# Kernel tuning notes

Measured on AMD Instinct MI355X. Metric: run time of the kernel, lower is better.

Reference implementation:

```python
import jax, jax.numpy as jnp
import numpy as np

B, S, E = 8, 2048, 128
DECAY = 1.2
LN_EPS = 1e-3  # keras LayerNormalization default epsilon


def setup_inputs() -> dict:
    key = jax.random.key(0)
    k1, k2, k3, k4 = jax.random.split(key, 4)
    return {
        "x": jax.random.normal(k1, (B, S, E), dtype=jnp.float32),
        "dense_w": jax.random.normal(k2, (E, E), dtype=jnp.float32) * 0.02,
        "dense_b": jnp.zeros((E,), dtype=jnp.float32),
        "concept_map": jax.random.normal(k3, (E, E, E), dtype=jnp.float32) * 0.02,
        "ln_gamma": jnp.ones((E,), dtype=jnp.float32),
        "ln_beta": jnp.zeros((E,), dtype=jnp.float32),
    }


def reference(x, dense_w, dense_b, concept_map, ln_gamma, ln_beta):
    # Dense projection
    h = x @ dense_w + dense_b  # (B, S, E)
    b, s, e = h.shape

    # Decayed prefix-sum recurrence: s_i = (s_{i-1} + h_{i-1}) / 1.2, s_0 = 0
    def step(carry, xt):
        new = (carry + xt) / DECAY
        return new, new

    h_t = jnp.swapaxes(h, 0, 1)  # (S, B, E)
    _, s_tail = jax.lax.scan(step, jnp.zeros((b, e), h.dtype), h_t[:-1])
    s_seq = jnp.concatenate([jnp.zeros((1, b, e), h.dtype), s_tail], axis=0)
    s_seq = jnp.swapaxes(s_seq, 0, 1)  # (B, S, E)

    # result[b,s,c] = sum_{a,p} h[b,s,a] * s_seq[b,s,p] * W[c,a,p]
    # (original code materializes (B,S,E,E,E); this is the fused contraction)
    out = jnp.einsum("bsa,bsp,cap->bsc", h, s_seq, concept_map)

    r = out + h
    # LayerNormalization over the last axis
    mean = jnp.mean(r, axis=-1, keepdims=True)
    var = jnp.var(r, axis=-1, keepdims=True)
    r = (r - mean) * jax.lax.rsqrt(var + LN_EPS) * ln_gamma + ln_beta
    # Dropout is identity at inference
    return r
```

## Files before the change

kernel.cpp:

```cpp
#include <hip/hip_runtime.h>
#include <hip/hip_bf16.h>
#include <math.h>

#define E_DIM 128
#define S_LEN 2048
#define B_N   8
#define BS    (B_N * S_LEN)
#define CHUNK 64
#define NCHUNK (S_LEN / CHUNK)

typedef unsigned short u16;
typedef _Float16 f16;
typedef _Float16 f16x2 __attribute__((ext_vector_type(2)));
typedef _Float16 f16x8 __attribute__((ext_vector_type(8)));
typedef float    f32x16 __attribute__((ext_vector_type(16)));

__global__ __launch_bounds__(256) void k_pre(const float* __restrict__ x,
                                             const float* __restrict__ dw,
                                             const float* __restrict__ db,
                                             const float* __restrict__ cm,
                                             float* __restrict__ hout,
                                             u16* __restrict__ wb) {
    if (blockIdx.x < 1024) {
        int t = blockIdx.x * 256 + threadIdx.x;
        int qs = t & 15, c = (t >> 4) & 127, a = t >> 11;
        const float* src = cm + (((long)(c << 7) + a) << 7) + ((qs ^ (c & 15)) << 3);
        float4 v0 = ((const float4*)src)[0];
        float4 v1 = ((const float4*)src)[1];
        union { f16 f[8]; uint4 v; } o;
        o.f[0] = (f16)v0.x; o.f[1] = (f16)v0.y; o.f[2] = (f16)v0.z; o.f[3] = (f16)v0.w;
        o.f[4] = (f16)v1.x; o.f[5] = (f16)v1.y; o.f[6] = (f16)v1.z; o.f[7] = (f16)v1.w;
        ((uint4*)wb)[t] = o.v;
        return;
    }
    __shared__ float Wl[E_DIM * E_DIM];
    const int t = threadIdx.x;
    const long r0 = (long)(blockIdx.x - 1024) * 64;

    float4* Wl4 = (float4*)Wl;
    const float4* w4 = (const float4*)dw;
#pragma unroll
    for (int i = 0; i < 16; ++i) Wl4[t + 256 * i] = w4[t + 256 * i];
    __syncthreads();

    const int cq = t & 31;
    const int rg = t >> 5;
    float4 bb = ((const float4*)db)[cq];
    float acc[8][4];
#pragma unroll
    for (int i = 0; i < 8; ++i) {
        acc[i][0] = bb.x; acc[i][1] = bb.y; acc[i][2] = bb.z; acc[i][3] = bb.w;
    }
#pragma unroll 4
    for (int k = 0; k < E_DIM; ++k) {
        float4 wv = Wl4[k * 32 + cq];
#pragma unroll
        for (int i = 0; i < 8; ++i) {
            float xv = x[(r0 + rg * 8 + i) * E_DIM + k];
            acc[i][0] += xv * wv.x;
            acc[i][1] += xv * wv.y;
            acc[i][2] += xv * wv.z;
            acc[i][3] += xv * wv.w;
        }
    }
    float4* h4 = (float4*)(hout + r0 * E_DIM);
#pragma unroll
    for (int i = 0; i < 8; ++i) {
        float4 o;
        o.x = acc[i][0]; o.y = acc[i][1]; o.z = acc[i][2]; o.w = acc[i][3];
        h4[(rg * 8 + i) * 32 + cq] = o;
    }
}

__global__ __launch_bounds__(128) void k_scan(const float* __restrict__ h,
                                              u16* __restrict__ sb16,
                                              float* __restrict__ fc,
                                              u16* __restrict__ hT) {
    const int b = blockIdx.x >> 5;
    const int j = blockIdx.x & 31;
    const int e = threadIdx.x;
    const float inv_d = (float)(1.0 / 1.2);
    const int pos0 = b * S_LEN + j * CHUNK;
    long base = (long)pos0 * E_DIM + e;
    float carry = 0.f;
    union { u16 u[8]; uint4 v; } hb;
#pragma unroll 1
    for (int i0 = 0; i0 < CHUNK; i0 += 8) {
#pragma unroll
        for (int k = 0; k < 8; ++k) {
            float hv = h[base + (long)(i0 + k) * E_DIM];
            union { f16 f; u16 u; } cu; cu.f = (f16)carry;
            sb16[base + (long)(i0 + k) * E_DIM] = cu.u;
            union { f16 f; u16 u; } hu; hu.f = (f16)hv;
            hb.u[k] = hu.u;
            carry = (carry + hv) * inv_d;
        }
        *(uint4*)&hT[(size_t)e * BS + pos0 + i0] = hb.v;
    }
    fc[(b * NCHUNK + j) * E_DIM + e] = carry;
}

__global__ __launch_bounds__(256, 2) void k_main(const u16* __restrict__ hT,
                                                 const u16* __restrict__ sb16,
                                                 const float* __restrict__ fc,
                                                 const u16* __restrict__ wb,
                                                 float* __restrict__ out,
                                                 float dm64) {
    __shared__ u16 Wl[2][16384];
    __shared__ float carr[2][E_DIM];
    const int t = threadIdx.x;
    const int w = t >> 6, l = t & 63;
    const int l31 = l & 31, hi = l >> 5;
    const int mb = blockIdx.x >> 2, r = blockIdx.x & 3;
    const int rbp = w >> 1, ntp = w & 1;

    const u16* wbK = wb + (size_t)(r * 32) * 16384;

#define STAGE(buf, sl) {                                                          \
    const u16* gsrc = wbK + (size_t)(sl) * 16384 + t * 8;                         \
    _Pragma("unroll")                                                             \
    for (int i = 0; i < 8; ++i)                                                   \
        __builtin_amdgcn_global_load_lds(                                         \
            (const __attribute__((address_space(1))) void*)(gsrc + i * 2048),     \
            (__attribute__((address_space(3))) void*)&Wl[buf][t * 8 + i * 2048],  \
            16, 0, 0); }

    STAGE(0, 0);

    const int row_base = mb * 128;
    const int bb = row_base >> 11;
    const int j0 = (row_base >> 6) & 31;
    {
        const int ch = t >> 7;
        const int e  = t & 127;
        const int jend = j0 + ch;
        float c = 0.f;
        for (int jj = 0; jj < jend; ++jj)
            c = fc[(bb * NCHUNK + jj) * E_DIM + e] + c * dm64;
        carr[ch][e] = c;
    }
    __syncthreads();

    const float L2D = 0.26303440583379383f;
    f16x2 s2[2][32];
#pragma unroll
    for (int rb = 0; rb < 2; ++rb) {
        const int row = row_base + rbp * 64 + rb * 32 + l31;
        const float f = exp2f(-L2D * (float)(row & 63));
        const uint4* sp = (const uint4*)(sb16 + (size_t)row * E_DIM + hi * 8);
#pragma unroll
        for (int ks = 0; ks < 8; ++ks) {
            union { uint4 u; u16 us[8]; } uu; uu.u = sp[ks * 2];
            const float* cp = &carr[rbp][ks * 16 + hi * 8];
#pragma unroll
            for (int q = 0; q < 4; ++q) {
                union { f16 f; u16 u; } a0; a0.u = uu.us[2 * q];
                union { f16 f; u16 u; } a1; a1.u = uu.us[2 * q + 1];
                f16x2 pr;
                pr.x = (f16)((float)a0.f + cp[2 * q] * f);
                pr.y = (f16)((float)a1.f + cp[2 * q + 1] * f);
                s2[rb][ks * 4 + q] = pr;
            }
        }
    }

    f32x16 acc[2][2];
#pragma unroll
    for (int rb = 0; rb < 2; ++rb)
#pragma unroll
        for (int nt = 0; nt < 2; ++nt)
#pragma unroll
            for (int g = 0; g < 16; ++g) acc[rb][nt][g] = 0.f;

    const u16* hTb = hT + (size_t)mb * 128 + rbp * 64 + l31;
    u16 h0 = hTb[(size_t)(r * 32) * BS];
    u16 h1 = hTb[(size_t)(r * 32) * BS + 32];

    const int sxb = l31 & 15;
    const int wcoff = (ntp * 64 + l31) * E_DIM;

#pragma unroll 1
    for (int sl = 0; sl < 32; ++sl) {
        const int cur = sl & 1;
        if (sl < 31) {
            if (cur) STAGE(0, sl + 1) else STAGE(1, sl + 1);
        }
        u16 nh0 = 0, nh1 = 0;
        if (sl < 31) {
            nh0 = hTb[(size_t)(r * 32 + sl + 1) * BS];
            nh1 = hTb[(size_t)(r * 32 + sl + 1) * BS + 32];
        }

        union { u16 u[2]; f16x2 v; } hu0, hu1;
        hu0.u[0] = h0; hu0.u[1] = h0;
        hu1.u[0] = h1; hu1.u[1] = h1;
        const u16* Wc = &Wl[cur][wcoff];
#pragma unroll
        for (int ks = 0; ks < 8; ++ks) {
            const int sx = ((ks << 1) + hi) ^ sxb;
            f16x8 b0 = *(const f16x8*)(Wc + sx * 8);
            f16x8 b1 = *(const f16x8*)(Wc + 32 * E_DIM + sx * 8);
            union { f16x2 h2[4]; f16x8 v; } a0, a1;
#pragma unroll
            for (int q = 0; q < 4; ++q) {
                a0.h2[q] = hu0.v * s2[0][ks * 4 + q];
                a1.h2[q] = hu1.v * s2[1][ks * 4 + q];
            }
            acc[0][0] = __builtin_amdgcn_mfma_f32_32x32x16_f16(a0.v, b0, acc[0][0], 0, 0, 0);
            acc[0][1] = __builtin_amdgcn_mfma_f32_32x32x16_f16(a0.v, b1, acc[0][1], 0, 0, 0);
            acc[1][0] = __builtin_amdgcn_mfma_f32_32x32x16_f16(a1.v, b0, acc[1][0], 0, 0, 0);
            acc[1][1] = __builtin_amdgcn_mfma_f32_32x32x16_f16(a1.v, b1, acc[1][1], 0, 0, 0);
        }
        h0 = nh0; h1 = nh1;
        __syncthreads();
    }
#undef STAGE

#pragma unroll
    for (int rb = 0; rb < 2; ++rb)
#pragma unroll
        for (int nt = 0; nt < 2; ++nt)
#pragma unroll
            for (int g = 0; g < 16; ++g) {
                int rowl = (g & 3) + 8 * (g >> 2) + 4 * hi;
                long row = (long)row_base + rbp * 64 + rb * 32 + rowl;
                int col = ntp * 64 + nt * 32 + l31;
                unsafeAtomicAdd(&out[row * E_DIM + col], acc[rb][nt][g]);
            }
}

__global__ __launch_bounds__(256) void k_ln(float* __restrict__ out,
                                            const float* __restrict__ h,
                                            const float* __restrict__ gamma,
                                            const float* __restrict__ beta) {
    const int t = threadIdx.x;
    const int l32 = t & 31, rl = t >> 5;
    const long row = (long)blockIdx.x * 8 + rl;
    float4 v  = ((const float4*)out)[row * 32 + l32];
    float4 hv = ((const float4*)h)[row * 32 + l32];
    v.x += hv.x; v.y += hv.y; v.z += hv.z; v.w += hv.w;
    float ls = v.x + v.y + v.z + v.w;
    float lq = v.x * v.x + v.y * v.y + v.z * v.z + v.w * v.w;
#pragma unroll
    for (int m = 1; m < 32; m <<= 1) {
        ls += __shfl_xor(ls, m, 64);
        lq += __shfl_xor(lq, m, 64);
    }
    float mean = ls * (1.f / 128.f);
    float var  = lq * (1.f / 128.f) - mean * mean;
    float inv  = rsqrtf(var + 1e-3f);
    float4 g = ((const float4*)gamma)[l32];
    float4 b = ((const float4*)beta)[l32];
    float4 o;
    o.x = (v.x - mean) * inv * g.x + b.x;
    o.y = (v.y - mean) * inv * g.y + b.y;
    o.z = (v.z - mean) * inv * g.z + b.z;
    o.w = (v.w - mean) * inv * g.w + b.w;
    ((float4*)out)[row * 32 + l32] = o;
}

extern "C" void kernel_launch(void* const* d_in, const int* in_sizes, int n_in,
                              void* d_out, int out_size, void* d_ws, size_t ws_size,
                              hipStream_t stream) {
    const float* x     = (const float*)d_in[0];
    const float* dw    = (const float*)d_in[1];
    const float* db    = (const float*)d_in[2];
    const float* cm    = (const float*)d_in[3];
    const float* gamma = (const float*)d_in[4];
    const float* beta  = (const float*)d_in[5];
    float* outp = (float*)d_out;

    float* ws = (float*)d_ws;
    float* h    = ws;
    float* fc   = ws + (size_t)BS * E_DIM;
    u16*   wb   = (u16*)(fc + B_N * NCHUNK * E_DIM);
    u16*   hT   = wb + (size_t)2097152;
    u16*   sb16 = hT + (size_t)BS * E_DIM;

    float dm64 = (float)pow(1.2, -64.0);

    hipMemsetAsync(d_out, 0, (size_t)BS * E_DIM * sizeof(float), stream);
    k_pre <<<dim3(1280), dim3(256), 0, stream>>>(x, dw, db, cm, h, wb);
    k_scan<<<dim3(B_N * NCHUNK), dim3(128), 0, stream>>>(h, sb16, fc, hT);
    k_main<<<dim3(512), dim3(256), 0, stream>>>(hT, sb16, fc, wb, outp, dm64);
    k_ln  <<<dim3(BS / 8), dim3(256), 0, stream>>>(outp, h, gamma, beta);
}
```

Baseline: 129.7 us.

## Enlarge k_main blocks to 512 threads with 4-deep W pipeline and LDS-staged h

Doubles the k_main block to 512 threads covering 256 rows, so each staged weight slice in LDS is shared by twice as many rows and the grid halves. Replaces the double buffer with a 4-slot ring that prefetches two slices ahead, using explicit vmcnt waits and a raw barrier instead of __syncthreads. All h values for the block's 32 slices are preloaded into LDS up front instead of per-iteration global loads, and MFMA sections run at raised wave priority. This adds LDS pressure (about 147KB per block), which may limit occupancy, and relies on hand-written waitcnt correctness.

```diff
diff --git a/kernel.cpp b/kernel.cpp
--- a/kernel.cpp
+++ b/kernel.cpp
@@ -100,44 +100,53 @@
     fc[(b * NCHUNK + j) * E_DIM + e] = carry;
 }
 
-__global__ __launch_bounds__(256, 2) void k_main(const u16* __restrict__ hT,
+__global__ __launch_bounds__(512, 2) void k_main(const u16* __restrict__ hT,
                                                  const u16* __restrict__ sb16,
                                                  const float* __restrict__ fc,
                                                  const u16* __restrict__ wb,
                                                  float* __restrict__ out,
                                                  float dm64) {
-    __shared__ u16 Wl[2][16384];
-    __shared__ float carr[2][E_DIM];
+    __shared__ u16 Wl[4][16384];
+    __shared__ u16 h16[32 * 256];
+    __shared__ float carr[4][E_DIM];
     const int t = threadIdx.x;
     const int w = t >> 6, l = t & 63;
     const int l31 = l & 31, hi = l >> 5;
     const int mb = blockIdx.x >> 2, r = blockIdx.x & 3;
-    const int rbp = w >> 1, ntp = w & 1;
+    const int rbp = w >> 1;
+    const int ntp = w & 1;
+    const int row_base = mb * 256;
 
     const u16* wbK = wb + (size_t)(r * 32) * 16384;
 
 #define STAGE(buf, sl) {                                                          \
     const u16* gsrc = wbK + (size_t)(sl) * 16384 + t * 8;                         \
     _Pragma("unroll")                                                             \
-    for (int i = 0; i < 8; ++i)                                                   \
+    for (int i = 0; i < 4; ++i)                                                   \
         __builtin_amdgcn_global_load_lds(                                         \
-            (const __attribute__((address_space(1))) void*)(gsrc + i * 2048),     \
-            (__attribute__((address_space(3))) void*)&Wl[buf][t * 8 + i * 2048],  \
+            (const __attribute__((address_space(1))) void*)(gsrc + i * 4096),     \
+            (__attribute__((address_space(3))) void*)&Wl[buf][t * 8 + i * 4096],  \
             16, 0, 0); }
 
     STAGE(0, 0);
-
-    const int row_base = mb * 128;
+    STAGE(1, 1);
+
     const int bb = row_base >> 11;
     const int j0 = (row_base >> 6) & 31;
     {
-        const int ch = t >> 7;
-        const int e  = t & 127;
-        const int jend = j0 + ch;
+        const int ch = t >> 7, e = t & 127;
         float c = 0.f;
-        for (int jj = 0; jj < jend; ++jj)
+        for (int jj = 0; jj < j0 + ch; ++jj)
             c = fc[(bb * NCHUNK + jj) * E_DIM + e] + c * dm64;
         carr[ch][e] = c;
+    }
+    {
+        const int al = t >> 4, rl0 = (t & 15) * 16;
+        const u16* src = hT + (size_t)(r * 32 + al) * BS + row_base + rl0;
+        uint4 v0 = ((const uint4*)src)[0];
+        uint4 v1 = ((const uint4*)src)[1];
+        *(uint4*)&h16[al * 256 + rl0] = v0;
+        *(uint4*)&h16[al * 256 + rl0 + 8] = v1;
     }
     __syncthreads();
 
@@ -172,29 +181,25 @@
 #pragma unroll
             for (int g = 0; g < 16; ++g) acc[rb][nt][g] = 0.f;
 
-    const u16* hTb = hT + (size_t)mb * 128 + rbp * 64 + l31;
-    u16 h0 = hTb[(size_t)(r * 32) * BS];
-    u16 h1 = hTb[(size_t)(r * 32) * BS + 32];
-
     const int sxb = l31 & 15;
     const int wcoff = (ntp * 64 + l31) * E_DIM;
+    const int hoff0 = rbp * 64 + l31;
 
 #pragma unroll 1
     for (int sl = 0; sl < 32; ++sl) {
-        const int cur = sl & 1;
-        if (sl < 31) {
-            if (cur) STAGE(0, sl + 1) else STAGE(1, sl + 1);
-        }
-        u16 nh0 = 0, nh1 = 0;
-        if (sl < 31) {
-            nh0 = hTb[(size_t)(r * 32 + sl + 1) * BS];
-            nh1 = hTb[(size_t)(r * 32 + sl + 1) * BS + 32];
-        }
-
+        if (sl < 30) { asm volatile("s_waitcnt vmcnt(4)" ::: "memory"); }
+        else         { asm volatile("s_waitcnt vmcnt(0)" ::: "memory"); }
+        __builtin_amdgcn_s_barrier();
+        if (sl < 30) { STAGE((sl + 2) & 3, sl + 2); }
+
+        u16 hv0 = h16[sl * 256 + hoff0];
+        u16 hv1 = h16[sl * 256 + hoff0 + 32];
         union { u16 u[2]; f16x2 v; } hu0, hu1;
-        hu0.u[0] = h0; hu0.u[1] = h0;
-        hu1.u[0] = h1; hu1.u[1] = h1;
-        const u16* Wc = &Wl[cur][wcoff];
+        hu0.u[0] = hv0; hu0.u[1] = hv0;
+        hu1.u[0] = hv1; hu1.u[1] = hv1;
+
+        const u16* Wc = &Wl[sl & 3][wcoff];
+        __builtin_amdgcn_s_setprio(1);
 #pragma unroll
         for (int ks = 0; ks < 8; ++ks) {
             const int sx = ((ks << 1) + hi) ^ sxb;
@@ -211,8 +216,7 @@
             acc[1][0] = __builtin_amdgcn_mfma_f32_32x32x16_f16(a1.v, b0, acc[1][0], 0, 0, 0);
             acc[1][1] = __builtin_amdgcn_mfma_f32_32x32x16_f16(a1.v, b1, acc[1][1], 0, 0, 0);
         }
-        h0 = nh0; h1 = nh1;
-        __syncthreads();
+        __builtin_amdgcn_s_setprio(0);
     }
 #undef STAGE
 
@@ -282,6 +286,6 @@
     hipMemsetAsync(d_out, 0, (size_t)BS * E_DIM * sizeof(float), stream);
     k_pre <<<dim3(1280), dim3(256), 0, stream>>>(x, dw, db, cm, h, wb);
     k_scan<<<dim3(B_N * NCHUNK), dim3(128), 0, stream>>>(h, sb16, fc, hT);
-    k_main<<<dim3(512), dim3(256), 0, stream>>>(hT, sb16, fc, wb, outp, dm64);
+    k_main<<<dim3(256), dim3(512), 0, stream>>>(hT, sb16, fc, wb, outp, dm64);
     k_ln  <<<dim3(BS / 8), dim3(256), 0, stream>>>(outp, h, gamma, beta);
 }
```

Measured after the change: 129.0 us. No clear change (-0.6%).

## Split main contraction into single-wave blocks reading weights directly into registers

Applied to the files above, without the earlier changes.

The main kernel is restructured from 512 four-wave blocks that double-buffer the weight slice in LDS into 4096 single-wave blocks. Each block handles one 32-column chunk and one half of the p dimension, and loads its pre-laid-out weight fragments straight into registers with a two-deep register pipeline. The weight pre-layout is changed to match the MFMA B-fragment order and drops the XOR swizzle. h values are staged in LDS, and the carry prefix is unrolled by four. This removes the LDS staging and block-wide barriers. In exchange it raises the number of atomic adds into the output and splits reuse across more blocks.

```diff
diff --git a/kernel.cpp b/kernel.cpp
--- a/kernel.cpp
+++ b/kernel.cpp
@@ -23,8 +23,10 @@
                                              u16* __restrict__ wb) {
     if (blockIdx.x < 1024) {
         int t = blockIdx.x * 256 + threadIdx.x;
-        int qs = t & 15, c = (t >> 4) & 127, a = t >> 11;
-        const float* src = cm + (((long)(c << 7) + a) << 7) + ((qs ^ (c & 15)) << 3);
+        int l31 = t & 31, hi = (t >> 5) & 1, ks = (t >> 6) & 7;
+        int cch = (t >> 9) & 3, a = t >> 11;
+        int c = cch * 32 + l31, qs = ks * 2 + hi;
+        const float* src = cm + (((long)(c << 7) + a) << 7) + (qs << 3);
         float4 v0 = ((const float4*)src)[0];
         float4 v1 = ((const float4*)src)[1];
         union { f16 f[8]; uint4 v; } o;
@@ -100,133 +102,140 @@
     fc[(b * NCHUNK + j) * E_DIM + e] = carry;
 }
 
-__global__ __launch_bounds__(256, 2) void k_main(const u16* __restrict__ hT,
-                                                 const u16* __restrict__ sb16,
-                                                 const float* __restrict__ fc,
-                                                 const u16* __restrict__ wb,
-                                                 float* __restrict__ out,
-                                                 float dm64) {
-    __shared__ u16 Wl[2][16384];
+__global__ __launch_bounds__(64, 2) void k_main(const u16* __restrict__ hT,
+                                                const u16* __restrict__ sb16,
+                                                const float* __restrict__ fc,
+                                                const u16* __restrict__ w2,
+                                                float* __restrict__ out,
+                                                float dm64) {
+    __shared__ u16 h16[32 * 128];
     __shared__ float carr[2][E_DIM];
-    const int t = threadIdx.x;
-    const int w = t >> 6, l = t & 63;
+    const int l = threadIdx.x;
     const int l31 = l & 31, hi = l >> 5;
-    const int mb = blockIdx.x >> 2, r = blockIdx.x & 3;
-    const int rbp = w >> 1, ntp = w & 1;
-
-    const u16* wbK = wb + (size_t)(r * 32) * 16384;
-
-#define STAGE(buf, sl) {                                                          \
-    const u16* gsrc = wbK + (size_t)(sl) * 16384 + t * 8;                         \
-    _Pragma("unroll")                                                             \
-    for (int i = 0; i < 8; ++i)                                                   \
-        __builtin_amdgcn_global_load_lds(                                         \
-            (const __attribute__((address_space(1))) void*)(gsrc + i * 2048),     \
-            (__attribute__((address_space(3))) void*)&Wl[buf][t * 8 + i * 2048],  \
-            16, 0, 0); }
-
-    STAGE(0, 0);
-
+
+    const int bid = blockIdx.x;
+    const int x = bid & 7, i = bid >> 3;
+    const int combo = x * 4 + (i >> 7);
+    const int mb  = i & 127;
+    const int cch = combo & 3;
+    const int r   = (combo >> 2) & 3;
+    const int kq  = combo >> 4;
     const int row_base = mb * 128;
+
+#pragma unroll
+    for (int it = 0; it < 8; ++it) {
+        int idx = it * 64 + l;
+        int al = idx >> 4, part = idx & 15;
+        const u16* src = hT + (size_t)(r * 32 + al) * BS + row_base + part * 8;
+        __builtin_amdgcn_global_load_lds(
+            (const __attribute__((address_space(1))) void*)src,
+            (__attribute__((address_space(3))) void*)&h16[idx * 8], 16, 0, 0);
+    }
+
     const int bb = row_base >> 11;
     const int j0 = (row_base >> 6) & 31;
+    const float L2D = 0.26303440583379383f;
     {
-        const int ch = t >> 7;
-        const int e  = t & 127;
-        const int jend = j0 + ch;
-        float c = 0.f;
-        for (int jj = 0; jj < jend; ++jj)
-            c = fc[(bb * NCHUNK + jj) * E_DIM + e] + c * dm64;
-        carr[ch][e] = c;
+        const float d2 = dm64 * dm64, d3 = d2 * dm64, d4 = d3 * dm64;
+#pragma unroll
+        for (int es = 0; es < 2; ++es) {
+            int e = l + es * 64;
+            const float* fp = fc + (size_t)(bb * NCHUNK) * E_DIM + e;
+            float c0 = 0.f;
+            int jj = 0;
+            for (; jj + 4 <= j0; jj += 4) {
+                float f0 = fp[(jj + 0) * E_DIM], f1 = fp[(jj + 1) * E_DIM];
+                float f2 = fp[(jj + 2) * E_DIM], f3 = fp[(jj + 3) * E_DIM];
+                c0 = c0 * d4 + f0 * d3 + f1 * d2 + f2 * dm64 + f3;
+            }
+            for (; jj < j0; ++jj) c0 = c0 * dm64 + fp[jj * E_DIM];
+            carr[0][e] = c0;
+            carr[1][e] = fp[j0 * E_DIM] + c0 * dm64;
+        }
     }
     __syncthreads();
 
-    const float L2D = 0.26303440583379383f;
-    f16x2 s2[2][32];
-#pragma unroll
-    for (int rb = 0; rb < 2; ++rb) {
-        const int row = row_base + rbp * 64 + rb * 32 + l31;
+    f16x2 s2[4][16];
+#pragma unroll
+    for (int rb = 0; rb < 4; ++rb) {
+        const int row = row_base + rb * 32 + l31;
         const float f = exp2f(-L2D * (float)(row & 63));
-        const uint4* sp = (const uint4*)(sb16 + (size_t)row * E_DIM + hi * 8);
-#pragma unroll
-        for (int ks = 0; ks < 8; ++ks) {
-            union { uint4 u; u16 us[8]; } uu; uu.u = sp[ks * 2];
-            const float* cp = &carr[rbp][ks * 16 + hi * 8];
+        const int ch = rb >> 1;
+#pragma unroll
+        for (int ksl = 0; ksl < 4; ++ksl) {
+            const int pbase = kq * 64 + ksl * 16 + hi * 8;
+            union { uint4 u; u16 us[8]; } uu;
+            uu.u = *(const uint4*)(sb16 + (size_t)row * E_DIM + pbase);
 #pragma unroll
             for (int q = 0; q < 4; ++q) {
                 union { f16 f; u16 u; } a0; a0.u = uu.us[2 * q];
                 union { f16 f; u16 u; } a1; a1.u = uu.us[2 * q + 1];
                 f16x2 pr;
-                pr.x = (f16)((float)a0.f + cp[2 * q] * f);
-                pr.y = (f16)((float)a1.f + cp[2 * q + 1] * f);
-                s2[rb][ks * 4 + q] = pr;
+                pr.x = (f16)((float)a0.f + carr[ch][pbase + 2 * q] * f);
+                pr.y = (f16)((float)a1.f + carr[ch][pbase + 2 * q + 1] * f);
+                s2[rb][ksl * 4 + q] = pr;
             }
         }
     }
 
-    f32x16 acc[2][2];
-#pragma unroll
-    for (int rb = 0; rb < 2; ++rb)
-#pragma unroll
-        for (int nt = 0; nt < 2; ++nt)
-#pragma unroll
-            for (int g = 0; g < 16; ++g) acc[rb][nt][g] = 0.f;
-
-    const u16* hTb = hT + (size_t)mb * 128 + rbp * 64 + l31;
-    u16 h0 = hTb[(size_t)(r * 32) * BS];
-    u16 h1 = hTb[(size_t)(r * 32) * BS + 32];
-
-    const int sxb = l31 & 15;
-    const int wcoff = (ntp * 64 + l31) * E_DIM;
+    f32x16 acc[4];
+#pragma unroll
+    for (int rb = 0; rb < 4; ++rb)
+#pragma unroll
+        for (int g = 0; g < 16; ++g) acc[rb][g] = 0.f;
+
+    const u16* wbase = w2 + (size_t)(r * 32) * 16384 + cch * 4096 + kq * 2048 + l * 8;
+
+#define LOADB(dst, sl) {                                                      \
+    const u16* _p = wbase + (size_t)(sl) * 16384;                             \
+    _Pragma("unroll")                                                         \
+    for (int _k = 0; _k < 4; ++_k) dst[_k] = *(const f16x8*)(_p + _k * 512); }
+
+#define LOADH(dst, sl) {                                                      \
+    _Pragma("unroll")                                                         \
+    for (int _rb = 0; _rb < 4; ++_rb) dst[_rb] = h16[(sl) * 128 + _rb * 32 + l31]; }
+
+#define COMPUTE(bf, hv)                                                       \
+    _Pragma("unroll")                                                         \
+    for (int _ksl = 0; _ksl < 4; ++_ksl) {                                    \
+        _Pragma("unroll")                                                     \
+        for (int _rb = 0; _rb < 4; ++_rb) {                                   \
+            union { u16 u[2]; f16x2 v; } _hh;                                 \
+            _hh.u[0] = hv[_rb]; _hh.u[1] = hv[_rb];                           \
+            union { f16x2 h2[4]; f16x8 v; } _A;                               \
+            _Pragma("unroll")                                                 \
+            for (int _q = 0; _q < 4; ++_q)                                    \
+                _A.h2[_q] = _hh.v * s2[_rb][_ksl * 4 + _q];                   \
+            acc[_rb] = __builtin_amdgcn_mfma_f32_32x32x16_f16(                \
+                _A.v, bf[_ksl], acc[_rb], 0, 0, 0);                           \
+        }                                                                     \
+    }
+
+    f16x8 bA[4], bB[4];
+    u16 hA[4], hB[4];
+    LOADB(bA, 0); LOADH(hA, 0);
 
 #pragma unroll 1
-    for (int sl = 0; sl < 32; ++sl) {
-        const int cur = sl & 1;
-        if (sl < 31) {
-            if (cur) STAGE(0, sl + 1) else STAGE(1, sl + 1);
-        }
-        u16 nh0 = 0, nh1 = 0;
-        if (sl < 31) {
-            nh0 = hTb[(size_t)(r * 32 + sl + 1) * BS];
-            nh1 = hTb[(size_t)(r * 32 + sl + 1) * BS + 32];
-        }
-
-        union { u16 u[2]; f16x2 v; } hu0, hu1;
-        hu0.u[0] = h0; hu0.u[1] = h0;
-        hu1.u[0] = h1; hu1.u[1] = h1;
-        const u16* Wc = &Wl[cur][wcoff];
-#pragma unroll
-        for (int ks = 0; ks < 8; ++ks) {
-            const int sx = ((ks << 1) + hi) ^ sxb;
-            f16x8 b0 = *(const f16x8*)(Wc + sx * 8);
-            f16x8 b1 = *(const f16x8*)(Wc + 32 * E_DIM + sx * 8);
-            union { f16x2 h2[4]; f16x8 v; } a0, a1;
-#pragma unroll
-            for (int q = 0; q < 4; ++q) {
-                a0.h2[q] = hu0.v * s2[0][ks * 4 + q];
-                a1.h2[q] = hu1.v * s2[1][ks * 4 + q];
-            }
-            acc[0][0] = __builtin_amdgcn_mfma_f32_32x32x16_f16(a0.v, b0, acc[0][0], 0, 0, 0);
-            acc[0][1] = __builtin_amdgcn_mfma_f32_32x32x16_f16(a0.v, b1, acc[0][1], 0, 0, 0);
-            acc[1][0] = __builtin_amdgcn_mfma_f32_32x32x16_f16(a1.v, b0, acc[1][0], 0, 0, 0);
-            acc[1][1] = __builtin_amdgcn_mfma_f32_32x32x16_f16(a1.v, b1, acc[1][1], 0, 0, 0);
-        }
-        h0 = nh0; h1 = nh1;
-        __syncthreads();
-    }
-#undef STAGE
-
-#pragma unroll
-    for (int rb = 0; rb < 2; ++rb)
-#pragma unroll
-        for (int nt = 0; nt < 2; ++nt)
-#pragma unroll
-            for (int g = 0; g < 16; ++g) {
-                int rowl = (g & 3) + 8 * (g >> 2) + 4 * hi;
-                long row = (long)row_base + rbp * 64 + rb * 32 + rowl;
-                int col = ntp * 64 + nt * 32 + l31;
-                unsafeAtomicAdd(&out[row * E_DIM + col], acc[rb][nt][g]);
-            }
+    for (int s2i = 0; s2i < 16; ++s2i) {
+        const int sl = s2i * 2;
+        LOADB(bB, sl + 1); LOADH(hB, sl + 1);
+        COMPUTE(bA, hA);
+        if (s2i < 15) { LOADB(bA, sl + 2); LOADH(hA, sl + 2); }
+        COMPUTE(bB, hB);
+    }
+#undef LOADB
+#undef LOADH
+#undef COMPUTE
+
+    const int col = cch * 32 + l31;
+#pragma unroll
+    for (int rb = 0; rb < 4; ++rb)
+#pragma unroll
+        for (int g = 0; g < 16; ++g) {
+            int rowl = (g & 3) + 8 * (g >> 2) + 4 * hi;
+            long row = (long)row_base + rb * 32 + rowl;
+            unsafeAtomicAdd(&out[row * E_DIM + col], acc[rb][g]);
+        }
 }
 
 __global__ __launch_bounds__(256) void k_ln(float* __restrict__ out,
@@ -282,6 +291,6 @@
     hipMemsetAsync(d_out, 0, (size_t)BS * E_DIM * sizeof(float), stream);
     k_pre <<<dim3(1280), dim3(256), 0, stream>>>(x, dw, db, cm, h, wb);
     k_scan<<<dim3(B_N * NCHUNK), dim3(128), 0, stream>>>(h, sb16, fc, hT);
-    k_main<<<dim3(512), dim3(256), 0, stream>>>(hT, sb16, fc, wb, outp, dm64);
+    k_main<<<dim3(4096), dim3(64), 0, stream>>>(hT, sb16, fc, wb, outp, dm64);
     k_ln  <<<dim3(BS / 8), dim3(256), 0, stream>>>(outp, h, gamma, beta);
 }
```

New measurement: 136.0 us. +4.9%, slower.
